# Performance work log

Hardware: AMD Instinct MI355X
Metric: run time of the kernel (lower is better)

Reference implementation:

```python
import jax, jax.numpy as jnp
import numpy as np

NUM_HEADS = 8
HIDDEN = 256


def _coattention(qf, rf, Wq, bq, Wk, bk, Wv, bv, Wo, bo, rel_emb):
    # qf, rf: (b, c, h, w); attention is axial over the height axis per width column.
    b, c, h, w = qf.shape
    T = rel_emb.shape[0]  # 2*max(h,w)-1
    q_in = qf.reshape(b, c, h * w).transpose(0, 2, 1)  # b (hw) c
    r_in = rf.reshape(b, c, h * w).transpose(0, 2, 1)
    q = (q_in @ Wq + bq).reshape(b, h, w, NUM_HEADS, HIDDEN).transpose(0, 3, 1, 2, 4)  # b n h w c
    k = (r_in @ Wk + bk).reshape(b, h, w, NUM_HEADS, HIDDEN).transpose(0, 3, 1, 2, 4)
    v = (r_in @ Wv + bv).reshape(b, h, w, NUM_HEADS, HIDDEN).transpose(0, 3, 1, 2, 4)
    scores = jnp.einsum('bnhwc,bnkwc->bnhwk', q, k)
    # relative index table: idx[i, j] = j - i, wrapped like torch negative indexing
    idx_h = (jnp.arange(h)[None, :] - jnp.arange(h)[:, None]) % T  # (h, h)
    idx_w = (jnp.arange(w)[None, :] - jnp.arange(w)[:, None]) % T  # (w, w); h == w required
    rel_h = rel_emb[idx_h]  # (h, h, c)
    rel_w = rel_emb[idx_w]  # (w, w, c)
    scores = scores + jnp.einsum('bnhwc,hkc->bnhwk', q, rel_h)
    scores = scores + jnp.einsum('bnhwc,wkc->bnhwk', q, rel_w)
    probs = jax.nn.softmax(scores / np.float32(np.sqrt(HIDDEN)), axis=-1)
    att = jnp.einsum('bnhwk,bnkwc->bnhwc', probs, v)
    out = att.transpose(0, 2, 3, 1, 4).reshape(b, h * w, NUM_HEADS * HIDDEN)  # b (hw) (n c)
    out = out @ Wo + bo
    return out.transpose(0, 2, 1).reshape(b, c, h, w)


def setup_inputs() -> dict:
    key = jax.random.key(0)
    ks = jax.random.split(key, 8)
    B, C, H, W = 4, 2048, 32, 32
    s = np.float32(0.02)
    return {
        'left_features': jax.random.normal(ks[0], (B, C, H, W), jnp.float32),
        'right_features': jax.random.normal(ks[1], (B, C, H, W), jnp.float32),
        'Wq': jax.random.normal(ks[2], (C, C), jnp.float32) * s,
        'bq': jnp.zeros((C,), jnp.float32),
        'Wk': jax.random.normal(ks[3], (C, C), jnp.float32) * s,
        'bk': jnp.zeros((C,), jnp.float32),
        'Wv': jax.random.normal(ks[4], (C, C), jnp.float32) * s,
        'bv': jnp.zeros((C,), jnp.float32),
        'Wo': jax.random.normal(ks[5], (C, C), jnp.float32) * s,
        'bo': jnp.zeros((C,), jnp.float32),
        'rel_emb': jax.random.normal(ks[6], (2 * max(H, W) - 1, HIDDEN), jnp.float32),
    }


def reference(left_features, right_features, Wq, bq, Wk, bk, Wv, bv, Wo, bo, rel_emb):
    weighted_r = _coattention(left_features, right_features, Wq, bq, Wk, bk, Wv, bv, Wo, bo, rel_emb)
    weighted_l = _coattention(right_features, left_features, Wq, bq, Wk, bk, Wv, bv, Wo, bo, rel_emb)
    left_attended = jnp.concatenate([left_features, weighted_r], axis=1)
    right_attended = jnp.concatenate([right_features, weighted_l], axis=1)
    return (left_attended, right_attended)
```

## Files before the change

### kernel.cpp

```cpp
#include <hip/hip_runtime.h>
#include <hip/hip_bf16.h>

typedef __attribute__((ext_vector_type(8))) short bf16x8;
typedef __attribute__((ext_vector_type(4))) float f32x4;

#define MFMA16(a, b, c) __builtin_amdgcn_mfma_f32_16x16x32_bf16((a), (b), (c), 0, 0, 0)

typedef __attribute__((address_space(1))) const void gconst_t;
typedef __attribute__((address_space(3))) void lds_t;
__device__ __forceinline__ void gload16(const void* gp, void* lp) {
    __builtin_amdgcn_global_load_lds((gconst_t*)gp, (lds_t*)lp, 16, 0, 0);
}

#define BAR() asm volatile("s_barrier" ::: "memory")
#define VMCNT4() asm volatile("s_waitcnt vmcnt(4)" ::: "memory")
#define VMCNT0() asm volatile("s_waitcnt vmcnt(0)" ::: "memory")
#define PRIO1() __builtin_amdgcn_s_setprio(1)
#define PRIO0() __builtin_amdgcn_s_setprio(0)

__global__ void transpose_cast(const float* __restrict__ in, __hip_bfloat16* __restrict__ out,
                               int R, int Ccols) {
    __shared__ float tile[32][33];
    int r0 = blockIdx.y * 32, c0 = blockIdx.x * 32;
    size_t zoff = (size_t)blockIdx.z * R * Ccols;
    const float* ib = in + zoff;
    __hip_bfloat16* ob = out + zoff;
    int tx = threadIdx.x, ty = threadIdx.y;
#pragma unroll
    for (int i = ty; i < 32; i += 8)
        tile[i][tx] = ib[(size_t)(r0 + i) * Ccols + c0 + tx];
    __syncthreads();
#pragma unroll
    for (int i = ty; i < 32; i += 8)
        ob[(size_t)(c0 + i) * R + r0 + tx] = __float2bfloat16(tile[tx][i]);
}

__global__ void conv_rel(const float* __restrict__ rel, __hip_bfloat16* __restrict__ relb) {
    int i = blockIdx.x * 256 + threadIdx.x;
    if (i < 64 * 256) {
        int r = i >> 8;
        relb[i] = __float2bfloat16(r < 63 ? rel[i] : 0.f);
    }
}

struct GArgs {
    const __hip_bfloat16* A[6];
    const __hip_bfloat16* B[6];
    void* C[6];
    const float* bias[6];
};

template <int MODE>
__global__ __launch_bounds__(512, 2) void gemm8p(GArgs ga, int N, int K,
                                                 float* __restrict__ dout) {
    __shared__ __align__(16) char smem[131072];

    const int gx = gridDim.x, gy = gridDim.y;
    int lid = blockIdx.x + gx * (blockIdx.y + gy * blockIdx.z);
    const int nwg = gx * gy * gridDim.z;
    int swz = (lid & 7) * (nwg >> 3) + (lid >> 3);
    const int z = swz / (gx * gy);
    int rem = swz - z * (gx * gy);
    const int by = rem / gx;
    const int bx = rem - by * gx;

    const __hip_bfloat16* __restrict__ A = ga.A[z];
    const __hip_bfloat16* __restrict__ B = ga.B[z];
    const float* __restrict__ bias = ga.bias[z];
    const int row0 = by * 256, col0 = bx * 256;

    const int tid = threadIdx.x;
    const int wave = tid >> 6, lane = tid & 63;
    const int l15 = lane & 15, lg = lane >> 4;
    const int wm = wave >> 2, wn = wave & 3;

    const int srow = tid >> 3;
    const int sch = (tid & 7) ^ (srow & 7);
    const int xr = (l15 & 7) << 4;
    const int off0 = (lg * 16) ^ xr;
    const int off1 = (64 + lg * 16) ^ xr;
    const int arow = wm * 16384;
    const int brow = 32768 + (wn >> 1) * 16384;
    const int bloc = (wn & 1) * 64;

    f32x4 acc[8][4] = {};
    bf16x8 a[4][2], bl[2][2], bh[2][2];

    const int NT = K >> 6;
    const int NI = NT >> 1;

    auto STAGE = [&](const __hip_bfloat16* base, int rowb, int T, int bufc, int isB, int h) {
#pragma unroll
        for (int L = 0; L < 2; ++L) {
            const __hip_bfloat16* g =
                base + (size_t)(rowb + h * 128 + L * 64 + srow) * K + T * 64 + sch * 8;
            gload16(g, smem + bufc * 65536 + isB * 32768 + h * 16384 + L * 8192 + wave * 1024);
        }
    };
    auto LDA = [&](int bufc, int mf, int ks) {
        return *(const bf16x8*)(smem + bufc * 65536 + arow + (mf * 16 + l15) * 128 +
                                (ks ? off1 : off0));
    };
    auto LDB = [&](int bufc, int nf, int ks) {
        return *(const bf16x8*)(smem + bufc * 65536 + brow + (bloc + nf * 16 + l15) * 128 +
                                (ks ? off1 : off0));
    };

#define READ_A(BUF, MOFF)                       \
    _Pragma("unroll") for (int mf = 0; mf < 4; ++mf) { \
        a[mf][0] = LDA(BUF, (MOFF) + mf, 0);    \
        a[mf][1] = LDA(BUF, (MOFF) + mf, 1);    \
    }
#define READ_B(BUF, NOFF, DST)                  \
    _Pragma("unroll") for (int nf = 0; nf < 2; ++nf) { \
        DST[nf][0] = LDB(BUF, (NOFF) + nf, 0);  \
        DST[nf][1] = LDB(BUF, (NOFF) + nf, 1);  \
    }
#define MFMA_QUAD(MOFF, NOFF, BR)                                                        \
    _Pragma("unroll") for (int mf = 0; mf < 4; ++mf)                                     \
    _Pragma("unroll") for (int nf = 0; nf < 2; ++nf) {                                   \
        acc[(MOFF) + mf][(NOFF) + nf] =                                                  \
            MFMA16(a[mf][0], BR[nf][0], acc[(MOFF) + mf][(NOFF) + nf]);                  \
        acc[(MOFF) + mf][(NOFF) + nf] =                                                  \
            MFMA16(a[mf][1], BR[nf][1], acc[(MOFF) + mf][(NOFF) + nf]);                  \
    }

    STAGE(B, col0, 0, 0, 1, 0);
    STAGE(A, row0, 0, 0, 0, 0);
    STAGE(A, row0, 0, 0, 0, 1);
    STAGE(B, col0, 0, 0, 1, 1);
    STAGE(B, col0, 1, 1, 1, 0);
    STAGE(A, row0, 1, 1, 0, 0);
    VMCNT4();
    BAR();

#pragma unroll 1
    for (int i = 0; i < NI; ++i) {
        const int t = 2 * i;
        const int T2 = (t + 2 < NT) ? t + 2 : t;
        const int T3 = (t + 3 < NT) ? t + 3 : t + 1;
        READ_A(0, 0); READ_B(0, 0, bl);
        STAGE(A, row0, t + 1, 1, 0, 1);
        BAR(); PRIO1(); MFMA_QUAD(0, 0, bl); PRIO0(); BAR();

        READ_B(0, 2, bh);
        STAGE(B, col0, t + 1, 1, 1, 1);
        BAR(); PRIO1(); MFMA_QUAD(0, 2, bh); PRIO0(); BAR();

        READ_A(0, 4);
        STAGE(B, col0, T2, 0, 1, 0);
        BAR(); PRIO1(); MFMA_QUAD(4, 2, bh); PRIO0(); BAR();

        STAGE(A, row0, T2, 0, 0, 0);
        BAR(); PRIO1(); MFMA_QUAD(4, 0, bl); PRIO0(); VMCNT4(); BAR();

        READ_A(1, 0); READ_B(1, 0, bl);
        STAGE(A, row0, T2, 0, 0, 1);
        BAR(); PRIO1(); MFMA_QUAD(0, 0, bl); PRIO0(); BAR();

        READ_B(1, 2, bh);
        STAGE(B, col0, T2, 0, 1, 1);
        BAR(); PRIO1(); MFMA_QUAD(0, 2, bh); PRIO0(); BAR();

        READ_A(1, 4);
        STAGE(B, col0, T3, 1, 1, 0);
        BAR(); PRIO1(); MFMA_QUAD(4, 2, bh); PRIO0(); BAR();

        STAGE(A, row0, T3, 1, 0, 0);
        BAR(); PRIO1(); MFMA_QUAD(4, 0, bl); PRIO0(); VMCNT4(); BAR();
    }
    VMCNT0();

    if (MODE == 0) {
        __hip_bfloat16* __restrict__ C = (__hip_bfloat16*)ga.C[z];
#pragma unroll
        for (int mf = 0; mf < 8; ++mf) {
            int m = row0 + wm * 128 + mf * 16 + lg * 4;
#pragma unroll
            for (int nf = 0; nf < 4; ++nf) {
                int n = col0 + wn * 64 + nf * 16 + l15;
                float bv = bias[n];
#pragma unroll
                for (int r = 0; r < 4; ++r)
                    C[(size_t)(m + r) * N + n] = __float2bfloat16(acc[mf][nf][r] + bv);
            }
        }
    } else {
        float* __restrict__ OB = dout + (size_t)z * 16777216;
#pragma unroll
        for (int mf = 0; mf < 8; ++mf) {
            int n0 = row0 + wm * 128 + mf * 16 + lg * 4;
#pragma unroll
            for (int nf = 0; nf < 4; ++nf) {
                int m = col0 + wn * 64 + nf * 16 + l15;
                size_t base = (size_t)(m >> 10) * 4194304 + (size_t)(m & 1023);
#pragma unroll
                for (int r = 0; r < 4; ++r) {
                    int n = n0 + r;
                    OB[base + (size_t)(2048 + n) * 1024] = acc[mf][nf][r] + bias[n];
                }
            }
        }
    }
#undef READ_A
#undef READ_B
#undef MFMA_QUAD
}

__global__ __launch_bounds__(256, 2) void attn_kernel(
    const __hip_bfloat16* __restrict__ Qa, const __hip_bfloat16* __restrict__ Ka,
    const __hip_bfloat16* __restrict__ Va, const __hip_bfloat16* __restrict__ Qb,
    const __hip_bfloat16* __restrict__ Kb, const __hip_bfloat16* __restrict__ Vb,
    const __hip_bfloat16* __restrict__ relb, __hip_bfloat16* __restrict__ Oa,
    __hip_bfloat16* __restrict__ Ob) {
    const int w = blockIdx.x;
    const int nh = blockIdx.y;
    const int zb = blockIdx.z;
    const int dir = zb >> 2, b = zb & 3;
    const __hip_bfloat16* __restrict__ Q = dir ? Qb : Qa;
    const __hip_bfloat16* __restrict__ K = dir ? Kb : Ka;
    const __hip_bfloat16* __restrict__ V = dir ? Vb : Va;
    __hip_bfloat16* __restrict__ O = dir ? Ob : Oa;

    __shared__ __align__(16) __hip_bfloat16 vt[256 * 40];
    __shared__ float ssc[32 * 32];
    __shared__ float es[32 * 64];
    __shared__ __align__(16) __hip_bfloat16 ps[32 * 32];

    const int tid = threadIdx.x;
    const int lane = tid & 63, wave = tid >> 6;
    const int l15 = lane & 15, lg = lane >> 4;
    const int mt = wave >> 1, nt = wave & 1;

    const size_t rowbase = ((size_t)b * 1024 + w) * 2048 + (size_t)nh * 256;

    for (int i = 0; i < 32; ++i) {
        int e = i * 256 + tid;
        int hk = e >> 8, c = e & 255;
        vt[c * 40 + hk] = V[rowbase + (size_t)hk * 65536 + c];
    }

    f32x4 sacc = {}, e0 = {}, e1 = {};
#pragma unroll
    for (int k8 = 0; k8 < 256; k8 += 32) {
        bf16x8 af = *(const bf16x8*)&Q[rowbase + (size_t)(mt * 16 + l15) * 65536 + k8 + lg * 8];
        bf16x8 bf = *(const bf16x8*)&K[rowbase + (size_t)(nt * 16 + l15) * 65536 + k8 + lg * 8];
        bf16x8 r0 = *(const bf16x8*)&relb[(size_t)(nt * 32 + l15) * 256 + k8 + lg * 8];
        bf16x8 r1 = *(const bf16x8*)&relb[(size_t)(nt * 32 + 16 + l15) * 256 + k8 + lg * 8];
        sacc = MFMA16(af, bf, sacc);
        e0 = MFMA16(af, r0, e0);
        e1 = MFMA16(af, r1, e1);
    }
#pragma unroll
    for (int r = 0; r < 4; ++r) {
        int row = mt * 16 + lg * 4 + r;
        ssc[row * 32 + nt * 16 + l15] = sacc[r];
        es[row * 64 + nt * 32 + l15] = e0[r];
        es[row * 64 + nt * 32 + 16 + l15] = e1[r];
    }
    __syncthreads();

    {
        int h = tid >> 3, sub = tid & 7;
        float v4[4];
        float mx = -1e30f;
#pragma unroll
        for (int i = 0; i < 4; ++i) {
            int k = sub * 4 + i;
            int dh = k - h; if (dh < 0) dh += 63;
            int dw = k - w; if (dw < 0) dw += 63;
            float s = (ssc[h * 32 + k] + es[h * 64 + dh] + es[h * 64 + dw]) * 0.0625f;
            v4[i] = s;
            mx = fmaxf(mx, s);
        }
        mx = fmaxf(mx, __shfl_xor(mx, 1));
        mx = fmaxf(mx, __shfl_xor(mx, 2));
        mx = fmaxf(mx, __shfl_xor(mx, 4));
        float sum = 0.f;
#pragma unroll
        for (int i = 0; i < 4; ++i) {
            v4[i] = __expf(v4[i] - mx);
            sum += v4[i];
        }
        sum += __shfl_xor(sum, 1);
        sum += __shfl_xor(sum, 2);
        sum += __shfl_xor(sum, 4);
        float inv = 1.f / sum;
#pragma unroll
        for (int i = 0; i < 4; ++i) ps[h * 32 + sub * 4 + i] = __float2bfloat16(v4[i] * inv);
    }
    __syncthreads();

    bf16x8 paf = *(const bf16x8*)&ps[(mt * 16 + l15) * 32 + lg * 8];
#pragma unroll
    for (int j = 0; j < 8; ++j) {
        int ct = nt * 8 + j;
        bf16x8 bv = *(const bf16x8*)&vt[(size_t)(ct * 16 + l15) * 40 + lg * 8];
        f32x4 oacc = {};
        oacc = MFMA16(paf, bv, oacc);
#pragma unroll
        for (int r = 0; r < 4; ++r) {
            int hh = mt * 16 + lg * 4 + r;
            O[rowbase + (size_t)hh * 65536 + ct * 16 + l15] = __float2bfloat16(oacc[r]);
        }
    }
}

__global__ void copy_feats(const float4* __restrict__ L, const float4* __restrict__ R,
                           float4* __restrict__ out) {
    int idx = blockIdx.x * 256 + threadIdx.x;
    int t = idx >= 2097152;
    int f4 = t ? idx - 2097152 : idx;
    int b = f4 >> 19, rem = f4 & 524287;
    float4 v = t ? R[f4] : L[f4];
    out[(size_t)t * 4194304 + (size_t)b * 1048576 + rem] = v;
}

extern "C" void kernel_launch(void* const* d_in, const int* in_sizes, int n_in, void* d_out,
                              int out_size, void* d_ws, size_t ws_size, hipStream_t stream) {
    const float* Xl = (const float*)d_in[0];
    const float* Xr = (const float*)d_in[1];
    const float* Wq = (const float*)d_in[2];
    const float* bq = (const float*)d_in[3];
    const float* Wk = (const float*)d_in[4];
    const float* bk = (const float*)d_in[5];
    const float* Wv = (const float*)d_in[6];
    const float* bv = (const float*)d_in[7];
    const float* Wo = (const float*)d_in[8];
    const float* bo = (const float*)d_in[9];
    const float* rel = (const float*)d_in[10];
    float* out = (float*)d_out;

    char* ws = (char*)d_ws;
    size_t off = 0;
    auto nxt = [&](size_t bytes) {
        void* p = ws + off;
        off += bytes;
        return p;
    };
    __hip_bfloat16* Xbl = (__hip_bfloat16*)nxt(16777216);
    __hip_bfloat16* Xbr = (__hip_bfloat16*)nxt(16777216);
    __hip_bfloat16* Wtq = (__hip_bfloat16*)nxt(8388608);
    __hip_bfloat16* Wtk = (__hip_bfloat16*)nxt(8388608);
    __hip_bfloat16* Wtv = (__hip_bfloat16*)nxt(8388608);
    __hip_bfloat16* Wto = (__hip_bfloat16*)nxt(8388608);
    __hip_bfloat16* relb = (__hip_bfloat16*)nxt(32768);
    __hip_bfloat16* Ql = (__hip_bfloat16*)nxt(16777216);
    __hip_bfloat16* Kl = (__hip_bfloat16*)nxt(16777216);
    __hip_bfloat16* Vl = (__hip_bfloat16*)nxt(16777216);
    __hip_bfloat16* Qr = (__hip_bfloat16*)nxt(16777216);
    __hip_bfloat16* Kr = (__hip_bfloat16*)nxt(16777216);
    __hip_bfloat16* Vr = (__hip_bfloat16*)nxt(16777216);
    __hip_bfloat16* At0 = Xbl;
    __hip_bfloat16* At1 = Xbr;

    dim3 tb(32, 8);
    transpose_cast<<<dim3(32, 64, 4), tb, 0, stream>>>(Xl, Xbl, 2048, 1024);
    transpose_cast<<<dim3(32, 64, 4), tb, 0, stream>>>(Xr, Xbr, 2048, 1024);
    transpose_cast<<<dim3(64, 64, 1), tb, 0, stream>>>(Wq, Wtq, 2048, 2048);
    transpose_cast<<<dim3(64, 64, 1), tb, 0, stream>>>(Wk, Wtk, 2048, 2048);
    transpose_cast<<<dim3(64, 64, 1), tb, 0, stream>>>(Wv, Wtv, 2048, 2048);
    transpose_cast<<<dim3(64, 64, 1), tb, 0, stream>>>(Wo, Wto, 2048, 2048);
    conv_rel<<<64, 256, 0, stream>>>(rel, relb);

    GArgs g1 = {};
    g1.A[0] = Xbl; g1.A[1] = Xbl; g1.A[2] = Xbl;
    g1.A[3] = Xbr; g1.A[4] = Xbr; g1.A[5] = Xbr;
    g1.B[0] = Wtq; g1.B[1] = Wtk; g1.B[2] = Wtv;
    g1.B[3] = Wtq; g1.B[4] = Wtk; g1.B[5] = Wtv;
    g1.C[0] = Ql; g1.C[1] = Kl; g1.C[2] = Vl;
    g1.C[3] = Qr; g1.C[4] = Kr; g1.C[5] = Vr;
    g1.bias[0] = bq; g1.bias[1] = bk; g1.bias[2] = bv;
    g1.bias[3] = bq; g1.bias[4] = bk; g1.bias[5] = bv;
    gemm8p<0><<<dim3(8, 16, 6), 512, 0, stream>>>(g1, 2048, 2048, nullptr);

    attn_kernel<<<dim3(32, 8, 8), 256, 0, stream>>>(Ql, Kr, Vr, Qr, Kl, Vl, relb, At0, At1);

    GArgs g2 = {};
    g2.A[0] = Wto; g2.A[1] = Wto;
    g2.B[0] = At0; g2.B[1] = At1;
    g2.bias[0] = bo; g2.bias[1] = bo;
    gemm8p<1><<<dim3(16, 8, 2), 512, 0, stream>>>(g2, 2048, 2048, out);

    copy_feats<<<16384, 256, 0, stream>>>((const float4*)Xl, (const float4*)Xr, (float4*)out);
}
```

Before: 366.6 us.

## Fuse feature copy into input transpose and remove GEMM loop barriers

The passthrough copy of the input features into the output is folded into the transpose/cast kernel. Each tile is written to the output in fp32 while it is already loaded, so the separate copy kernel and its second read of the inputs are gone. Separately, the GEMM main loop drops the trailing barrier after each MFMA quad and moves the vmcnt wait ahead of the barrier, halving barrier count per step. This risks LDS read/write races between waves if the staging schedule relied on those barriers.

```diff
diff --git a/kernel.cpp b/kernel.cpp
--- a/kernel.cpp
+++ b/kernel.cpp
@@ -19,16 +19,26 @@
 #define PRIO0() __builtin_amdgcn_s_setprio(0)
 
 __global__ void transpose_cast(const float* __restrict__ in, __hip_bfloat16* __restrict__ out,
-                               int R, int Ccols) {
+                               int R, int Ccols, float* __restrict__ copy_out) {
     __shared__ float tile[32][33];
     int r0 = blockIdx.y * 32, c0 = blockIdx.x * 32;
     size_t zoff = (size_t)blockIdx.z * R * Ccols;
     const float* ib = in + zoff;
     __hip_bfloat16* ob = out + zoff;
     int tx = threadIdx.x, ty = threadIdx.y;
-#pragma unroll
-    for (int i = ty; i < 32; i += 8)
-        tile[i][tx] = ib[(size_t)(r0 + i) * Ccols + c0 + tx];
+    if (copy_out) {
+        float* cb = copy_out + (size_t)blockIdx.z * 4194304;
+#pragma unroll
+        for (int i = ty; i < 32; i += 8) {
+            float v = ib[(size_t)(r0 + i) * Ccols + c0 + tx];
+            tile[i][tx] = v;
+            cb[(size_t)(r0 + i) * Ccols + c0 + tx] = v;
+        }
+    } else {
+#pragma unroll
+        for (int i = ty; i < 32; i += 8)
+            tile[i][tx] = ib[(size_t)(r0 + i) * Ccols + c0 + tx];
+    }
     __syncthreads();
 #pragma unroll
     for (int i = ty; i < 32; i += 8)
@@ -141,33 +151,35 @@
         const int T3 = (t + 3 < NT) ? t + 3 : t + 1;
         READ_A(0, 0); READ_B(0, 0, bl);
         STAGE(A, row0, t + 1, 1, 0, 1);
-        BAR(); PRIO1(); MFMA_QUAD(0, 0, bl); PRIO0(); BAR();
+        BAR(); PRIO1(); MFMA_QUAD(0, 0, bl); PRIO0();
 
         READ_B(0, 2, bh);
         STAGE(B, col0, t + 1, 1, 1, 1);
-        BAR(); PRIO1(); MFMA_QUAD(0, 2, bh); PRIO0(); BAR();
+        BAR(); PRIO1(); MFMA_QUAD(0, 2, bh); PRIO0();
 
         READ_A(0, 4);
         STAGE(B, col0, T2, 0, 1, 0);
-        BAR(); PRIO1(); MFMA_QUAD(4, 2, bh); PRIO0(); BAR();
+        BAR(); PRIO1(); MFMA_QUAD(4, 2, bh); PRIO0();
 
         STAGE(A, row0, T2, 0, 0, 0);
-        BAR(); PRIO1(); MFMA_QUAD(4, 0, bl); PRIO0(); VMCNT4(); BAR();
+        VMCNT4();
+        BAR(); PRIO1(); MFMA_QUAD(4, 0, bl); PRIO0();
 
         READ_A(1, 0); READ_B(1, 0, bl);
         STAGE(A, row0, T2, 0, 0, 1);
-        BAR(); PRIO1(); MFMA_QUAD(0, 0, bl); PRIO0(); BAR();
+        BAR(); PRIO1(); MFMA_QUAD(0, 0, bl); PRIO0();
 
         READ_B(1, 2, bh);
         STAGE(B, col0, T2, 0, 1, 1);
-        BAR(); PRIO1(); MFMA_QUAD(0, 2, bh); PRIO0(); BAR();
+        BAR(); PRIO1(); MFMA_QUAD(0, 2, bh); PRIO0();
 
         READ_A(1, 4);
         STAGE(B, col0, T3, 1, 1, 0);
-        BAR(); PRIO1(); MFMA_QUAD(4, 2, bh); PRIO0(); BAR();
+        BAR(); PRIO1(); MFMA_QUAD(4, 2, bh); PRIO0();
 
         STAGE(A, row0, T3, 1, 0, 0);
-        BAR(); PRIO1(); MFMA_QUAD(4, 0, bl); PRIO0(); VMCNT4(); BAR();
+        VMCNT4();
+        BAR(); PRIO1(); MFMA_QUAD(4, 0, bl); PRIO0();
     }
     VMCNT0();
 
@@ -304,16 +316,6 @@
             O[rowbase + (size_t)hh * 65536 + ct * 16 + l15] = __float2bfloat16(oacc[r]);
         }
     }
-}
-
-__global__ void copy_feats(const float4* __restrict__ L, const float4* __restrict__ R,
-                           float4* __restrict__ out) {
-    int idx = blockIdx.x * 256 + threadIdx.x;
-    int t = idx >= 2097152;
-    int f4 = t ? idx - 2097152 : idx;
-    int b = f4 >> 19, rem = f4 & 524287;
-    float4 v = t ? R[f4] : L[f4];
-    out[(size_t)t * 4194304 + (size_t)b * 1048576 + rem] = v;
 }
 
 extern "C" void kernel_launch(void* const* d_in, const int* in_sizes, int n_in, void* d_out,
@@ -355,12 +357,12 @@
     __hip_bfloat16* At1 = Xbr;
 
     dim3 tb(32, 8);
-    transpose_cast<<<dim3(32, 64, 4), tb, 0, stream>>>(Xl, Xbl, 2048, 1024);
-    transpose_cast<<<dim3(32, 64, 4), tb, 0, stream>>>(Xr, Xbr, 2048, 1024);
-    transpose_cast<<<dim3(64, 64, 1), tb, 0, stream>>>(Wq, Wtq, 2048, 2048);
-    transpose_cast<<<dim3(64, 64, 1), tb, 0, stream>>>(Wk, Wtk, 2048, 2048);
-    transpose_cast<<<dim3(64, 64, 1), tb, 0, stream>>>(Wv, Wtv, 2048, 2048);
-    transpose_cast<<<dim3(64, 64, 1), tb, 0, stream>>>(Wo, Wto, 2048, 2048);
+    transpose_cast<<<dim3(32, 64, 4), tb, 0, stream>>>(Xl, Xbl, 2048, 1024, out);
+    transpose_cast<<<dim3(32, 64, 4), tb, 0, stream>>>(Xr, Xbr, 2048, 1024, out + 16777216);
+    transpose_cast<<<dim3(64, 64, 1), tb, 0, stream>>>(Wq, Wtq, 2048, 2048, nullptr);
+    transpose_cast<<<dim3(64, 64, 1), tb, 0, stream>>>(Wk, Wtk, 2048, 2048, nullptr);
+    transpose_cast<<<dim3(64, 64, 1), tb, 0, stream>>>(Wv, Wtv, 2048, 2048, nullptr);
+    transpose_cast<<<dim3(64, 64, 1), tb, 0, stream>>>(Wo, Wto, 2048, 2048, nullptr);
     conv_rel<<<64, 256, 0, stream>>>(rel, relb);
 
     GArgs g1 = {};
@@ -381,6 +383,4 @@
     g2.B[0] = At0; g2.B[1] = At1;
     g2.bias[0] = bo; g2.bias[1] = bo;
     gemm8p<1><<<dim3(16, 8, 2), 512, 0, stream>>>(g2, 2048, 2048, out);
-
-    copy_feats<<<16384, 256, 0, stream>>>((const float4*)Xl, (const float4*)Xr, (float4*)out);
-}
+}
```

After: 353.8 us. -3.5%, faster.
